# Optimization experiments

Hardware: AMD Instinct MI355X
Metric: run time of the kernel (lower is better)

Reference implementation:

```python
import jax, jax.numpy as jnp
import numpy as np

EPS = 1e-8  # LayerNorm eps used throughout SFSRec


def _ln(x, g, b):
    m = x.mean(-1, keepdims=True)
    v = ((x - m) ** 2).mean(-1, keepdims=True)  # biased variance, as torch LayerNorm
    return (x - m) * jax.lax.rsqrt(v + EPS) * g + b


def setup_inputs() -> dict:
    key = jax.random.key(0)
    ks = jax.random.split(key, 16)
    B, L, H, V, NB = 16, 200, 256, 50000, 2
    std = 0.02  # initializer_range
    input_ids = jax.random.randint(ks[0], (B, L), 0, V + 1)
    item_emb = jax.random.normal(ks[1], (V + 1, H), jnp.float32) * std
    item_emb = item_emb.at[0].set(0.0)  # padding_idx row zeroed
    pos_emb = jax.random.normal(ks[2], (L, H), jnp.float32) * std  # maxlen == L
    emb_g = jnp.ones((H,), jnp.float32)
    emb_b = jnp.zeros((H,), jnp.float32)
    Wv = jax.random.normal(ks[3], (NB, H, H), jnp.float32) * std  # value_proj (out,in)
    Wo = jax.random.normal(ks[4], (NB, H, H), jnp.float32) * std  # out_proj (out,in)
    attn_g = jnp.ones((NB, H), jnp.float32)
    attn_b = jnp.zeros((NB, H), jnp.float32)
    W1 = jax.random.normal(ks[5], (NB, H, H), jnp.float32) * std  # conv1 kernel=1 -> linear
    b1 = jnp.zeros((NB, H), jnp.float32)
    W2 = jax.random.normal(ks[6], (NB, H, H), jnp.float32) * std
    b2 = jnp.zeros((NB, H), jnp.float32)
    ffn_g = jnp.ones((NB, H), jnp.float32)
    ffn_b = jnp.zeros((NB, H), jnp.float32)
    return {"input_ids": input_ids, "item_emb": item_emb, "pos_emb": pos_emb,
            "emb_g": emb_g, "emb_b": emb_b, "Wv": Wv, "Wo": Wo,
            "attn_g": attn_g, "attn_b": attn_b, "W1": W1, "b1": b1,
            "W2": W2, "b2": b2, "ffn_g": ffn_g, "ffn_b": ffn_b}


def reference(input_ids, item_emb, pos_emb, emb_g, emb_b, Wv, Wo,
              attn_g, attn_b, W1, b1, W2, b2, ffn_g, ffn_b):
    B, L = input_ids.shape
    H = item_emb.shape[1]
    x = item_emb[input_ids] * jnp.sqrt(jnp.float32(H)) + pos_emb[None, :, :]
    x = _ln(x, emb_g, emb_b)
    keep = (input_ids != 0)[..., None].astype(x.dtype)  # timeline mask
    x = x * keep
    # causal uniform average: T @ v == cumsum(v)/count -> O(L*H) instead of O(L^2*H)
    inv_counts = (1.0 / jnp.arange(1, L + 1, dtype=x.dtype))[None, :, None]
    NB = Wv.shape[0]
    for i in range(NB):
        v = jnp.einsum('blh,oh->blo', jnp.einsum('blh,oh->blo', x, Wv[i]), Wo[i])
        mixed = jnp.cumsum(v, axis=1) * inv_counts
        x = _ln(x + mixed, attn_g[i], attn_b[i]) * keep
        y = jax.nn.relu(jnp.einsum('blh,oh->blo', x, W1[i]) + b1[i])
        y = jnp.einsum('blh,oh->blo', y, W2[i]) + b2[i]
        x = _ln(x + y, ffn_g[i], ffn_b[i]) * keep
    # add_head: logits over all items (last_layernorm is NOT applied in the original forward)
    return jnp.einsum('blh,vh->blv', x, item_emb)
```

## Files before the change

### kernel.cpp

```cpp
#include <hip/hip_runtime.h>

#define H 256
#define LSEQ 200
#define NB 16
#define BL 3200
#define V1 50001
#define NPAD 50048

#define GAS __attribute__((address_space(1)))
#define LAS __attribute__((address_space(3)))

typedef __attribute__((ext_vector_type(8))) short short8;
typedef __attribute__((ext_vector_type(4))) float f32x4;

__device__ __forceinline__ unsigned short f2bf(float f) {
    unsigned int u = __builtin_bit_cast(unsigned int, f);
    u += 0x7fffu + ((u >> 16) & 1u);
    return (unsigned short)(u >> 16);
}


__global__ void k_f32_to_bf16(const float* __restrict__ src,
                              unsigned short* __restrict__ dst, int n) {
    int i = blockIdx.x * blockDim.x + threadIdx.x;
    if (i < n) dst[i] = f2bf(src[i]);
}

__global__ void k_wc(const float* __restrict__ Wo, const float* __restrict__ Wv,
                     unsigned short* __restrict__ Wc) {
    int i = blockIdx.y;
    int o = blockIdx.x;
    int h = threadIdx.x;
    const float* wo = Wo + ((size_t)i * H + o) * H;
    const float* wv = Wv + (size_t)i * H * H + h;
    float acc = 0.0f;
#pragma unroll 8
    for (int m = 0; m < H; ++m) acc = fmaf(wo[m], wv[(size_t)m * H], acc);
    Wc[((size_t)i * H + o) * H + h] = f2bf(acc);
}

__global__ void k_conv_emb(const float* __restrict__ src, unsigned short* __restrict__ dst) {
    size_t i4 = (size_t)blockIdx.x * blockDim.x + threadIdx.x;
    size_t total4 = (size_t)NPAD * H / 4;
    if (i4 >= total4) return;
    size_t e0 = i4 * 4;
    size_t row = e0 >> 8;
    ushort4 o;
    if (row < V1) {
        float4 v = *(const float4*)(src + e0);
        o.x = f2bf(v.x); o.y = f2bf(v.y); o.z = f2bf(v.z); o.w = f2bf(v.w);
    } else {
        o.x = o.y = o.z = o.w = 0;
    }
    *(ushort4*)(dst + e0) = o;
}


__device__ __forceinline__ void block_reduce2(float& s, float& ss, float* red) {
#pragma unroll
    for (int off = 32; off > 0; off >>= 1) {
        s += __shfl_down(s, off);
        ss += __shfl_down(ss, off);
    }
    int t = threadIdx.x;
    if ((t & 63) == 0) { red[(t >> 6) * 2] = s; red[(t >> 6) * 2 + 1] = ss; }
    __syncthreads();
    s  = red[0] + red[2] + red[4] + red[6];
    ss = red[1] + red[3] + red[5] + red[7];
}

__global__ __launch_bounds__(256) void k_embed_ln(
    const int* __restrict__ ids, const float* __restrict__ emb,
    const float* __restrict__ pos, const float* __restrict__ g,
    const float* __restrict__ bta, float* __restrict__ xf,
    unsigned short* __restrict__ xb) {
    __shared__ float red[8];
    int bl = blockIdx.x;
    int h = threadIdx.x;
    int l = bl % LSEQ;
    int id = ids[bl];
    float val = emb[(size_t)id * H + h] * 16.0f + pos[(size_t)l * H + h];
    float s = val, ss = val * val;
    block_reduce2(s, ss, red);
    float mean = s * (1.0f / H);
    float var = fmaxf(ss * (1.0f / H) - mean * mean, 0.0f);
    float rs = rsqrtf(var + 1e-8f);
    float keep = (id != 0) ? 1.0f : 0.0f;
    float o = ((val - mean) * rs * g[h] + bta[h]) * keep;
    xf[(size_t)bl * H + h] = o;
    xb[(size_t)bl * H + h] = f2bf(o);
}

__global__ __launch_bounds__(256) void k_add_ln(
    const float* __restrict__ x, const float* __restrict__ d,
    const float* __restrict__ g, const float* __restrict__ bta,
    const int* __restrict__ ids, float* __restrict__ xf,
    unsigned short* __restrict__ xb) {
    __shared__ float red[8];
    int bl = blockIdx.x;
    int h = threadIdx.x;
    float val = x[(size_t)bl * H + h] + d[(size_t)bl * H + h];
    float s = val, ss = val * val;
    block_reduce2(s, ss, red);
    float mean = s * (1.0f / H);
    float var = fmaxf(ss * (1.0f / H) - mean * mean, 0.0f);
    float rs = rsqrtf(var + 1e-8f);
    float keep = (ids[bl] != 0) ? 1.0f : 0.0f;
    float o = ((val - mean) * rs * g[h] + bta[h]) * keep;
    xf[(size_t)bl * H + h] = o;
    xb[(size_t)bl * H + h] = f2bf(o);
}

__global__ void k_cumsum(float* __restrict__ v) {
    int b = blockIdx.x, h = threadIdx.x;
    float* p = v + (size_t)b * LSEQ * H + h;
    float acc = 0.0f;
    for (int l = 0; l < LSEQ; ++l) {
        acc += p[(size_t)l * H];
        p[(size_t)l * H] = acc * (1.0f / (float)(l + 1));
    }
}

template<int BIAS, int RELU, int WF32, int WBF16>
__global__ __launch_bounds__(256) void k_gemm64(
    const unsigned short* __restrict__ A,
    const unsigned short* __restrict__ Bmat,
    const float* __restrict__ bias,
    float* __restrict__ outF,
    unsigned short* __restrict__ outB,
    int N, int K) {
    int bm = blockIdx.x * 64;
    int bn = blockIdx.y * 64;
    int tid = threadIdx.x;
    int w = tid >> 6, l = tid & 63;
    int wr = (w >> 1) * 32, wc = (w & 1) * 32;
    int l16 = l & 15, lk = (l >> 4) * 8;

    const unsigned short* Ap = A + (size_t)(bm + wr + l16) * K + lk;
    const unsigned short* Bp = Bmat + (size_t)(bn + wc + l16) * K + lk;

    f32x4 acc00 = {0.f,0.f,0.f,0.f}, acc01 = {0.f,0.f,0.f,0.f};
    f32x4 acc10 = {0.f,0.f,0.f,0.f}, acc11 = {0.f,0.f,0.f,0.f};

#pragma unroll
    for (int k0 = 0; k0 < 256; k0 += 32) {
        short8 a0 = *(const short8*)(Ap + k0);
        short8 a1 = *(const short8*)(Ap + (size_t)16 * K + k0);
        short8 b0 = *(const short8*)(Bp + k0);
        short8 b1 = *(const short8*)(Bp + (size_t)16 * K + k0);
        acc00 = __builtin_amdgcn_mfma_f32_16x16x32_bf16(a0, b0, acc00, 0, 0, 0);
        acc01 = __builtin_amdgcn_mfma_f32_16x16x32_bf16(a0, b1, acc01, 0, 0, 0);
        acc10 = __builtin_amdgcn_mfma_f32_16x16x32_bf16(a1, b0, acc10, 0, 0, 0);
        acc11 = __builtin_amdgcn_mfma_f32_16x16x32_bf16(a1, b1, acc11, 0, 0, 0);
    }

    int r0 = (l >> 4) * 4;
#pragma unroll
    for (int i = 0; i < 2; ++i) {
#pragma unroll
        for (int j = 0; j < 2; ++j) {
            f32x4 a = (i == 0) ? (j == 0 ? acc00 : acc01) : (j == 0 ? acc10 : acc11);
            int col = bn + wc + j * 16 + l16;
            float bv = BIAS ? bias[col] : 0.0f;
            int rowb = bm + wr + i * 16 + r0;
#pragma unroll
            for (int r = 0; r < 4; ++r) {
                float vv = a[r] + bv;
                if (RELU) vv = fmaxf(vv, 0.0f);
                size_t idx = (size_t)(rowb + r) * N + col;
                if (WF32) outF[idx] = vv;
                if (WBF16) outB[idx] = f2bf(vv);
            }
        }
    }
}

#define LGM 25
#define LGN 391
#define LGWG (LGM * LGN)

__global__ __launch_bounds__(256, 3) void k_logits(
    const unsigned short* __restrict__ A,
    const unsigned short* __restrict__ B,
    float* __restrict__ out) {
    __shared__ unsigned short lA[2][128 * 32];
    __shared__ unsigned short lB[2][128 * 32];

    int orig = blockIdx.x;
    int q = LGWG >> 3, r = LGWG & 7;
    int xcd = orig & 7, sub = orig >> 3;
    int wg = (xcd < r ? xcd * (q + 1) : r * (q + 1) + (xcd - r) * q) + sub;
    int mi = wg % LGM, ni = wg / LGM;
    int bm = mi * 128, bn = ni * 128;

    int tid = threadIdx.x;
    int w = tid >> 6, l = tid & 63;
    int wr = (w >> 1) * 64, wc = (w & 1) * 64;
    int l16 = l & 15, lc = l >> 4;

    f32x4 acc[4][4] = {};

    auto stage = [&](int buf, int kt) {
        int k0 = kt * 32;
#pragma unroll
        for (int rr = 0; rr < 2; ++rr) {
            int t = tid + rr * 256;
            int row = t >> 2;
            int cd = t & 3;
            int cs = cd ^ (row & 3);
            unsigned short* lpA = &lA[buf][(t & ~63) * 8];
            unsigned short* lpB = &lB[buf][(t & ~63) * 8];
            const unsigned short* gA = A + (size_t)(bm + row) * 256 + k0 + cs * 8;
            const unsigned short* gB = B + (size_t)(bn + row) * 256 + k0 + cs * 8;
            __builtin_amdgcn_global_load_lds((const GAS unsigned int*)gA,
                                             (LAS unsigned int*)lpA, 16, 0, 0);
            __builtin_amdgcn_global_load_lds((const GAS unsigned int*)gB,
                                             (LAS unsigned int*)lpB, 16, 0, 0);
        }
    };

    int buf = 0;
    stage(0, 0);
    __syncthreads();

#pragma unroll
    for (int kt = 0; kt < 8; ++kt) {
        if (kt < 7) stage(buf ^ 1, kt + 1);
        short8 af[4], bf[4];
#pragma unroll
        for (int i = 0; i < 4; ++i) {
            int rowA = wr + i * 16 + l16;
            af[i] = *(const short8*)&lA[buf][rowA * 32 + ((lc ^ (rowA & 3)) * 8)];
            int rowB = wc + i * 16 + l16;
            bf[i] = *(const short8*)&lB[buf][rowB * 32 + ((lc ^ (rowB & 3)) * 8)];
        }
#pragma unroll
        for (int i = 0; i < 4; ++i)
#pragma unroll
            for (int j = 0; j < 4; ++j)
                acc[i][j] = __builtin_amdgcn_mfma_f32_16x16x32_bf16(
                    af[i], bf[j], acc[i][j], 0, 0, 0);
        __syncthreads();
        buf ^= 1;
    }

#pragma unroll
    for (int i = 0; i < 4; ++i) {
        int mrow = bm + wr + i * 16 + lc * 4;
#pragma unroll
        for (int j = 0; j < 4; ++j) {
            int n = bn + wc + j * 16 + l16;
            if (n < V1) {
#pragma unroll
                for (int rg = 0; rg < 4; ++rg)
                    out[(size_t)(mrow + rg) * V1 + n] = acc[i][j][rg];
            }
        }
    }
}


extern "C" void kernel_launch(void* const* d_in, const int* in_sizes, int n_in,
                              void* d_out, int out_size, void* d_ws, size_t ws_size,
                              hipStream_t stream) {
    const int*   ids      = (const int*)d_in[0];
    const float* item_emb = (const float*)d_in[1];
    const float* pos_emb  = (const float*)d_in[2];
    const float* emb_g    = (const float*)d_in[3];
    const float* emb_b    = (const float*)d_in[4];
    const float* Wv       = (const float*)d_in[5];
    const float* Wo       = (const float*)d_in[6];
    const float* attn_g   = (const float*)d_in[7];
    const float* attn_b   = (const float*)d_in[8];
    const float* W1       = (const float*)d_in[9];
    const float* b1       = (const float*)d_in[10];
    const float* W2       = (const float*)d_in[11];
    const float* b2       = (const float*)d_in[12];
    const float* ffn_g    = (const float*)d_in[13];
    const float* ffn_b    = (const float*)d_in[14];
    float* out = (float*)d_out;

    char* ws = (char*)d_ws;
    size_t off = 0;
    auto alloc = [&](size_t bytes) -> void* {
        void* p = ws + off;
        off += (bytes + 255) & ~(size_t)255;
        return p;
    };
    float* xf  = (float*)alloc((size_t)BL * H * 4);
    float* vbuf= (float*)alloc((size_t)BL * H * 4);
    float* y2  = (float*)alloc((size_t)BL * H * 4);
    unsigned short* xb  = (unsigned short*)alloc((size_t)BL * H * 2);
    unsigned short* y1b = (unsigned short*)alloc((size_t)BL * H * 2);
    unsigned short* WcB = (unsigned short*)alloc((size_t)2 * H * H * 2);
    unsigned short* W1B = (unsigned short*)alloc((size_t)2 * H * H * 2);
    unsigned short* W2B = (unsigned short*)alloc((size_t)2 * H * H * 2);
    unsigned short* embB= (unsigned short*)alloc((size_t)NPAD * H * 2);

    k_f32_to_bf16<<<dim3(512), dim3(256), 0, stream>>>(W1, W1B, 2 * H * H);
    k_f32_to_bf16<<<dim3(512), dim3(256), 0, stream>>>(W2, W2B, 2 * H * H);
    k_wc<<<dim3(H, 2), dim3(H), 0, stream>>>(Wo, Wv, WcB);
    {
        int n4 = NPAD * H / 4;
        k_conv_emb<<<dim3((n4 + 255) / 256), dim3(256), 0, stream>>>(item_emb, embB);
    }

    k_embed_ln<<<dim3(BL), dim3(H), 0, stream>>>(ids, item_emb, pos_emb, emb_g, emb_b, xf, xb);

    for (int i = 0; i < 2; ++i) {
        k_gemm64<0,0,1,0><<<dim3(BL / 64, H / 64), dim3(256), 0, stream>>>(
            xb, WcB + (size_t)i * H * H, nullptr, vbuf, nullptr, H, H);
        k_cumsum<<<dim3(NB), dim3(H), 0, stream>>>(vbuf);
        k_add_ln<<<dim3(BL), dim3(H), 0, stream>>>(
            xf, vbuf, attn_g + (size_t)i * H, attn_b + (size_t)i * H, ids, xf, xb);
        k_gemm64<1,1,0,1><<<dim3(BL / 64, H / 64), dim3(256), 0, stream>>>(
            xb, W1B + (size_t)i * H * H, b1 + (size_t)i * H, nullptr, y1b, H, H);
        k_gemm64<1,0,1,0><<<dim3(BL / 64, H / 64), dim3(256), 0, stream>>>(
            y1b, W2B + (size_t)i * H * H, b2 + (size_t)i * H, y2, nullptr, H, H);
        k_add_ln<<<dim3(BL), dim3(H), 0, stream>>>(
            xf, y2, ffn_g + (size_t)i * H, ffn_b + (size_t)i * H, ids, xf, xb);
    }

    k_logits<<<dim3(LGWG), dim3(256), 0, stream>>>(xb, embB, out);
}
```

Before: 423.4 us.

## Preload full B tile in LDS for logits, MFMA weight fusion, split cumsum

The logits kernel now loads the entire 128x256 embedding tile into LDS once and keeps all A fragments in registers, removing the per-k double-buffer and barriers at the cost of 64KB LDS and lower occupancy (launch bounds 3 to 2). The Wo·Wv weight product moves from a scalar per-thread dot-product kernel to a transpose plus the existing bf16 MFMA GEMM. The cumsum is split across 4x more blocks with a 4-way manually unrolled loop to expose more parallelism.

```diff
diff --git a/kernel.cpp b/kernel.cpp
--- a/kernel.cpp
+++ b/kernel.cpp
@@ -26,17 +26,19 @@
     if (i < n) dst[i] = f2bf(src[i]);
 }
 
-__global__ void k_wc(const float* __restrict__ Wo, const float* __restrict__ Wv,
-                     unsigned short* __restrict__ Wc) {
-    int i = blockIdx.y;
-    int o = blockIdx.x;
-    int h = threadIdx.x;
-    const float* wo = Wo + ((size_t)i * H + o) * H;
-    const float* wv = Wv + (size_t)i * H * H + h;
-    float acc = 0.0f;
-#pragma unroll 8
-    for (int m = 0; m < H; ++m) acc = fmaf(wo[m], wv[(size_t)m * H], acc);
-    Wc[((size_t)i * H + o) * H + h] = f2bf(acc);
+__global__ __launch_bounds__(256) void k_transpose_bf(
+    const float* __restrict__ src, unsigned short* __restrict__ dst) {
+    __shared__ float t[32][33];
+    int i = blockIdx.z;
+    int m0 = blockIdx.x * 32, h0 = blockIdx.y * 32;
+    int tx = threadIdx.x & 31, ty = threadIdx.x >> 5;
+#pragma unroll
+    for (int s = 0; s < 32; s += 8)
+        t[ty + s][tx] = src[((size_t)i * 256 + m0 + ty + s) * 256 + h0 + tx];
+    __syncthreads();
+#pragma unroll
+    for (int s = 0; s < 32; s += 8)
+        dst[((size_t)i * 256 + h0 + ty + s) * 256 + m0 + tx] = f2bf(t[tx][ty + s]);
 }
 
 __global__ void k_conv_emb(const float* __restrict__ src, unsigned short* __restrict__ dst) {
@@ -111,13 +113,20 @@
     xb[(size_t)bl * H + h] = f2bf(o);
 }
 
-__global__ void k_cumsum(float* __restrict__ v) {
-    int b = blockIdx.x, h = threadIdx.x;
+__global__ __launch_bounds__(64) void k_cumsum(float* __restrict__ v) {
+    int b = blockIdx.x;
+    int h = blockIdx.y * 64 + threadIdx.x;
     float* p = v + (size_t)b * LSEQ * H + h;
     float acc = 0.0f;
-    for (int l = 0; l < LSEQ; ++l) {
-        acc += p[(size_t)l * H];
-        p[(size_t)l * H] = acc * (1.0f / (float)(l + 1));
+    for (int l = 0; l < LSEQ; l += 4) {
+        float a0 = p[(size_t)(l + 0) * H];
+        float a1 = p[(size_t)(l + 1) * H];
+        float a2 = p[(size_t)(l + 2) * H];
+        float a3 = p[(size_t)(l + 3) * H];
+        acc += a0; p[(size_t)(l + 0) * H] = acc * (1.0f / (float)(l + 1));
+        acc += a1; p[(size_t)(l + 1) * H] = acc * (1.0f / (float)(l + 2));
+        acc += a2; p[(size_t)(l + 2) * H] = acc * (1.0f / (float)(l + 3));
+        acc += a3; p[(size_t)(l + 3) * H] = acc * (1.0f / (float)(l + 4));
     }
 }
 
@@ -179,12 +188,11 @@
 #define LGN 391
 #define LGWG (LGM * LGN)
 
-__global__ __launch_bounds__(256, 3) void k_logits(
+__global__ __launch_bounds__(256, 2) void k_logits(
     const unsigned short* __restrict__ A,
     const unsigned short* __restrict__ B,
     float* __restrict__ out) {
-    __shared__ unsigned short lA[2][128 * 32];
-    __shared__ unsigned short lB[2][128 * 32];
+    __shared__ unsigned short lB[128 * 256];
 
     int orig = blockIdx.x;
     int q = LGWG >> 3, r = LGWG & 7;
@@ -198,50 +206,44 @@
     int wr = (w >> 1) * 64, wc = (w & 1) * 64;
     int l16 = l & 15, lc = l >> 4;
 
+#pragma unroll
+    for (int it = 0; it < 16; ++it) {
+        int idx = it * 256 + tid;
+        int row = idx >> 5;
+        int cd = idx & 31;
+        int cs = cd ^ (row & 7);
+        const unsigned short* g = B + (size_t)(bn + row) * 256 + cs * 8;
+        unsigned short* lp = &lB[(idx & ~63) * 8];
+        __builtin_amdgcn_global_load_lds((const GAS unsigned int*)g,
+                                         (LAS unsigned int*)lp, 16, 0, 0);
+    }
+
+    short8 af[8][4];
+#pragma unroll
+    for (int kt = 0; kt < 8; ++kt)
+#pragma unroll
+        for (int i = 0; i < 4; ++i)
+            af[kt][i] = *(const short8*)(A + (size_t)(bm + wr + i * 16 + l16) * 256
+                                           + kt * 32 + lc * 8);
+
+    __syncthreads();
+
     f32x4 acc[4][4] = {};
-
-    auto stage = [&](int buf, int kt) {
-        int k0 = kt * 32;
-#pragma unroll
-        for (int rr = 0; rr < 2; ++rr) {
-            int t = tid + rr * 256;
-            int row = t >> 2;
-            int cd = t & 3;
-            int cs = cd ^ (row & 3);
-            unsigned short* lpA = &lA[buf][(t & ~63) * 8];
-            unsigned short* lpB = &lB[buf][(t & ~63) * 8];
-            const unsigned short* gA = A + (size_t)(bm + row) * 256 + k0 + cs * 8;
-            const unsigned short* gB = B + (size_t)(bn + row) * 256 + k0 + cs * 8;
-            __builtin_amdgcn_global_load_lds((const GAS unsigned int*)gA,
-                                             (LAS unsigned int*)lpA, 16, 0, 0);
-            __builtin_amdgcn_global_load_lds((const GAS unsigned int*)gB,
-                                             (LAS unsigned int*)lpB, 16, 0, 0);
-        }
-    };
-
-    int buf = 0;
-    stage(0, 0);
-    __syncthreads();
-
 #pragma unroll
     for (int kt = 0; kt < 8; ++kt) {
-        if (kt < 7) stage(buf ^ 1, kt + 1);
-        short8 af[4], bf[4];
-#pragma unroll
-        for (int i = 0; i < 4; ++i) {
-            int rowA = wr + i * 16 + l16;
-            af[i] = *(const short8*)&lA[buf][rowA * 32 + ((lc ^ (rowA & 3)) * 8)];
-            int rowB = wc + i * 16 + l16;
-            bf[i] = *(const short8*)&lB[buf][rowB * 32 + ((lc ^ (rowB & 3)) * 8)];
+        short8 bf[4];
+#pragma unroll
+        for (int j = 0; j < 4; ++j) {
+            int row = wc + j * 16 + l16;
+            int pc = (kt * 4 + lc) ^ (row & 7);
+            bf[j] = *(const short8*)&lB[row * 256 + pc * 8];
         }
 #pragma unroll
         for (int i = 0; i < 4; ++i)
 #pragma unroll
             for (int j = 0; j < 4; ++j)
                 acc[i][j] = __builtin_amdgcn_mfma_f32_16x16x32_bf16(
-                    af[i], bf[j], acc[i][j], 0, 0, 0);
-        __syncthreads();
-        buf ^= 1;
+                    af[kt][i], bf[j], acc[i][j], 0, 0, 0);
     }
 
 #pragma unroll
@@ -295,22 +297,29 @@
     unsigned short* WcB = (unsigned short*)alloc((size_t)2 * H * H * 2);
     unsigned short* W1B = (unsigned short*)alloc((size_t)2 * H * H * 2);
     unsigned short* W2B = (unsigned short*)alloc((size_t)2 * H * H * 2);
+    unsigned short* WoB = (unsigned short*)alloc((size_t)2 * H * H * 2);
+    unsigned short* WvT = (unsigned short*)alloc((size_t)2 * H * H * 2);
     unsigned short* embB= (unsigned short*)alloc((size_t)NPAD * H * 2);
 
     k_f32_to_bf16<<<dim3(512), dim3(256), 0, stream>>>(W1, W1B, 2 * H * H);
     k_f32_to_bf16<<<dim3(512), dim3(256), 0, stream>>>(W2, W2B, 2 * H * H);
-    k_wc<<<dim3(H, 2), dim3(H), 0, stream>>>(Wo, Wv, WcB);
+    k_f32_to_bf16<<<dim3(512), dim3(256), 0, stream>>>(Wo, WoB, 2 * H * H);
+    k_transpose_bf<<<dim3(8, 8, 2), dim3(256), 0, stream>>>(Wv, WvT);
     {
         int n4 = NPAD * H / 4;
         k_conv_emb<<<dim3((n4 + 255) / 256), dim3(256), 0, stream>>>(item_emb, embB);
     }
+    for (int i = 0; i < 2; ++i)
+        k_gemm64<0,0,0,1><<<dim3(4, 4), dim3(256), 0, stream>>>(
+            WoB + (size_t)i * H * H, WvT + (size_t)i * H * H, nullptr,
+            nullptr, WcB + (size_t)i * H * H, H, H);
 
     k_embed_ln<<<dim3(BL), dim3(H), 0, stream>>>(ids, item_emb, pos_emb, emb_g, emb_b, xf, xb);
 
     for (int i = 0; i < 2; ++i) {
         k_gemm64<0,0,1,0><<<dim3(BL / 64, H / 64), dim3(256), 0, stream>>>(
             xb, WcB + (size_t)i * H * H, nullptr, vbuf, nullptr, H, H);
-        k_cumsum<<<dim3(NB), dim3(H), 0, stream>>>(vbuf);
+        k_cumsum<<<dim3(NB, 4), dim3(64), 0, stream>>>(vbuf);
         k_add_ln<<<dim3(BL), dim3(H), 0, stream>>>(
             xf, vbuf, attn_g + (size_t)i * H, attn_b + (size_t)i * H, ids, xf, xb);
         k_gemm64<1,1,0,1><<<dim3(BL / 64, H / 64), dim3(256), 0, stream>>>(
```

Result: slower. 447.3 us (+5.6%).
